# Optimization experiments

Measured on AMD Instinct MI355X. Metric: run time of the kernel, lower is better.

## Reference

```python
import jax, jax.numpy as jnp
import numpy as np

B, C, H, W = 16, 256, 64, 64
DIM = 8
HEADS = C // DIM          # 32
TD = HEADS * DIM          # 256 (total_dim)
EPS = 1e-15
BN_EPS = 1e-5


def setup_inputs() -> dict:
    key = jax.random.key(0)
    ks = jax.random.split(key, 7)
    s = 0.05
    return {
        "x": jax.random.normal(ks[0], (B, C, H, W), jnp.float32),
        "w_qkv": jax.random.normal(ks[1], (3 * TD, C), jnp.float32) * s,
        "w_dw": jax.random.normal(ks[2], (3 * TD, 1, 5, 5), jnp.float32) * s,
        "w_pw": jax.random.normal(ks[3], (3 * TD, DIM), jnp.float32) * s,
        "w_proj": jax.random.normal(ks[4], (C, 2 * TD), jnp.float32) * s,
        "bn_gamma": jnp.ones((C,), jnp.float32),
        "bn_beta": jnp.zeros((C,), jnp.float32),
        "bn_mean": jax.random.normal(ks[5], (C,), jnp.float32) * 0.1,
        "bn_var": jax.random.uniform(ks[6], (C,), jnp.float32, 0.5, 1.5),
    }


def reference(x, w_qkv, w_dw, w_pw, w_proj, bn_gamma, bn_beta, bn_mean, bn_var):
    # qkv: 1x1 conv, no bias -> (B, 3*TD, H, W)
    qkv = jnp.einsum('bchw,oc->bohw', x, w_qkv)

    # multi-scale aggregation: 5x5 depthwise conv then grouped 1x1 conv (groups = 3*HEADS)
    dw = jax.lax.conv_general_dilated(
        qkv, w_dw, window_strides=(1, 1), padding=[(2, 2), (2, 2)],
        dimension_numbers=('NCHW', 'OIHW', 'NCHW'), feature_group_count=3 * TD)
    G = 3 * HEADS                                   # groups; DIM channels per group
    dwg = dw.reshape(B, G, DIM, H, W)
    wg = w_pw.reshape(G, DIM, DIM)                  # (group, out_per_group, in_per_group)
    agg = jnp.einsum('bgihw,goi->bgohw', dwg, wg).reshape(B, 3 * TD, H, W)

    qkv_ms = jnp.concatenate([qkv, agg], axis=1)    # (B, 6*TD, H, W)

    # ReLU linear attention (H*W > dim branch)
    h2 = qkv_ms.shape[1] // (3 * DIM)               # 2*HEADS effective heads
    t = qkv_ms.reshape(B, h2, 3 * DIM, H * W)
    q = jax.nn.relu(t[:, :, :DIM])                  # (B,h2,DIM,N)
    k = jax.nn.relu(t[:, :, DIM:2 * DIM])           # (B,h2,DIM,N)
    v = t[:, :, 2 * DIM:]                           # (B,h2,DIM,N)
    v = jnp.concatenate([v, jnp.ones_like(v[:, :, :1])], axis=2)  # pad ones row -> (B,h2,DIM+1,N)

    vk = jnp.einsum('bhen,bhdn->bhed', v, k)        # (B,h2,DIM+1,DIM)
    out = jnp.einsum('bhed,bhdn->bhen', vk, q)      # (B,h2,DIM+1,N)
    out = out[:, :, :-1] / (out[:, :, -1:] + EPS)   # normalize by padded-ones channel
    out = out.reshape(B, h2 * DIM, H, W)            # (B, 2*TD, H, W)

    # proj: 1x1 conv + BatchNorm (inference stats)
    y = jnp.einsum('bchw,oc->bohw', out, w_proj)
    scale = (bn_gamma / jnp.sqrt(bn_var + BN_EPS))[None, :, None, None]
    y = (y - bn_mean[None, :, None, None]) * scale + bn_beta[None, :, None, None]

    return x + y
```

## Files before the change

### kernel.cpp

```cpp
#include <hip/hip_runtime.h>

#define BB 16
#define CC 256
#define HW 4096
#define TD3 768
#define TD2 512
#define WQ_N (TD3 * CC)
#define WP_N (CC * TD2)

typedef __bf16 bf16x8 __attribute__((ext_vector_type(8)));
typedef float f32x4 __attribute__((ext_vector_type(4)));
typedef const __attribute__((address_space(1))) unsigned int glb_u32;
typedef __attribute__((address_space(3))) unsigned int lds_u32;

__device__ inline ushort f2bf(float f) {
    union { float f; uint u; } v; v.f = f;
    uint u = v.u;
    return (ushort)((u + 0x7FFFu + ((u >> 16) & 1u)) >> 16);
}
__device__ inline float bf2f(ushort h) {
    union { uint u; float f; } v; v.u = ((uint)h) << 16;
    return v.f;
}
__device__ inline uint pack2(float a, float b) {
    return (uint)f2bf(a) | ((uint)f2bf(b) << 16);
}

__launch_bounds__(256)
__global__ void k_prep(const float* __restrict__ w_qkv, const float* __restrict__ w_proj,
                       ushort* __restrict__ wq_hi, ushort* __restrict__ wq_lo,
                       ushort* __restrict__ wp_hi, ushort* __restrict__ wp_lo) {
    int i = blockIdx.x * 256 + threadIdx.x;
    if (i < WQ_N) {
        float f = w_qkv[i];
        ushort h = f2bf(f);
        wq_hi[i] = h;
        wq_lo[i] = f2bf(f - bf2f(h));
    }
    if (i < WP_N) {
        float f = w_proj[i];
        ushort h = f2bf(f);
        wp_hi[i] = h;
        wp_lo[i] = f2bf(f - bf2f(h));
    }
}

__launch_bounds__(256)
__global__ void k0_transpose(const float* __restrict__ x, ushort* __restrict__ x_cl) {
    __shared__ float tile[64][65];
    int b = blockIdx.z;
    int n0 = blockIdx.x * 64;
    int c0 = blockIdx.y * 64;
    int t = threadIdx.x;
    const float* xp = x + ((size_t)b * CC + c0) * HW + n0;
    int nl = t & 63;
    int cl0 = t >> 6;
#pragma unroll
    for (int i = 0; i < 16; i++) {
        int cl = cl0 + i * 4;
        tile[cl][nl] = xp[(size_t)cl * HW + nl];
    }
    __syncthreads();
#pragma unroll
    for (int it = 0; it < 2; it++) {
        int item = t + it * 256;
        int n = item >> 3;
        int cc = item & 7;
        uint4 o;
        o.x = pack2(tile[cc * 8 + 0][n], tile[cc * 8 + 1][n]);
        o.y = pack2(tile[cc * 8 + 2][n], tile[cc * 8 + 3][n]);
        o.z = pack2(tile[cc * 8 + 4][n], tile[cc * 8 + 5][n]);
        o.w = pack2(tile[cc * 8 + 6][n], tile[cc * 8 + 7][n]);
        *(uint4*)(x_cl + ((size_t)b * HW + n0 + n) * CC + c0 + cc * 8) = o;
    }
}

__launch_bounds__(256)
__global__ void k1_qkv(const ushort* __restrict__ x_cl, const ushort* __restrict__ wq_hi,
                       const ushort* __restrict__ wq_lo, float* __restrict__ qkv_pl) {
    __shared__ ushort Ald[128][32];
    __shared__ ushort Bh[128][32];
    __shared__ ushort Bl[128][32];
    int b = blockIdx.z;
    int n0 = blockIdx.x * 128;
    int o0 = blockIdx.y * 128;
    int t = threadIdx.x;
    int w = t >> 6, l = t & 63;
    int wn = (w >> 1) * 64, wo = (w & 1) * 64;
    f32x4 acc[4][4];
#pragma unroll
    for (int m = 0; m < 4; m++)
#pragma unroll
        for (int o = 0; o < 4; o++)
#pragma unroll
            for (int r = 0; r < 4; r++) acc[m][o][r] = 0.f;

    const ushort* Ap  = x_cl + ((size_t)b * HW + n0) * CC;
    const ushort* Bph = wq_hi + (size_t)o0 * CC;
    const ushort* Bpl = wq_lo + (size_t)o0 * CC;
    int rowl = (l >> 2);
    int coll = (l & 3) * 8;

    for (int k0 = 0; k0 < CC; k0 += 32) {
#pragma unroll
        for (int i = 0; i < 2; i++) {
            int rbase = w * 32 + i * 16;
            int row = rbase + rowl;
            __builtin_amdgcn_global_load_lds((glb_u32*)(Ap + (size_t)row * CC + k0 + coll),
                                             (lds_u32*)&Ald[rbase][0], 16, 0, 0);
            __builtin_amdgcn_global_load_lds((glb_u32*)(Bph + (size_t)row * CC + k0 + coll),
                                             (lds_u32*)&Bh[rbase][0], 16, 0, 0);
            __builtin_amdgcn_global_load_lds((glb_u32*)(Bpl + (size_t)row * CC + k0 + coll),
                                             (lds_u32*)&Bl[rbase][0], 16, 0, 0);
        }
        __syncthreads();
        bf16x8 af[4], bh[4], bl[4];
#pragma unroll
        for (int m = 0; m < 4; m++) af[m] = *(const bf16x8*)&Ald[wn + m * 16 + (l & 15)][(l >> 4) * 8];
#pragma unroll
        for (int o = 0; o < 4; o++) {
            bh[o] = *(const bf16x8*)&Bh[wo + o * 16 + (l & 15)][(l >> 4) * 8];
            bl[o] = *(const bf16x8*)&Bl[wo + o * 16 + (l & 15)][(l >> 4) * 8];
        }
#pragma unroll
        for (int m = 0; m < 4; m++)
#pragma unroll
            for (int o = 0; o < 4; o++) {
                acc[m][o] = __builtin_amdgcn_mfma_f32_16x16x32_bf16(af[m], bh[o], acc[m][o], 0, 0, 0);
                acc[m][o] = __builtin_amdgcn_mfma_f32_16x16x32_bf16(af[m], bl[o], acc[m][o], 0, 0, 0);
            }
        __syncthreads();
    }
#pragma unroll
    for (int m = 0; m < 4; m++) {
        int nb = n0 + wn + m * 16 + (l >> 4) * 4;
#pragma unroll
        for (int oi = 0; oi < 4; oi++) {
            int o = o0 + wo + oi * 16 + (l & 15);
            float4 v4 = {acc[m][oi][0], acc[m][oi][1], acc[m][oi][2], acc[m][oi][3]};
            *(float4*)(qkv_pl + ((size_t)b * TD3 + o) * HW + nb) = v4;
        }
    }
}

__launch_bounds__(256)
__global__ void k2_dwpw(const float* __restrict__ qkv_pl, const float* __restrict__ w_dw,
                        const float* __restrict__ w_pw, float* __restrict__ agg_pl) {
    __shared__ __align__(16) float lds[2][36][76];
    int g = blockIdx.x;
    int strip = blockIdx.y;
    int b = blockIdx.z;
    int t = threadIdx.x;
    int y0 = strip * 32;
    const float* wg  = w_dw + (size_t)g * 200;
    const float* wpg = w_pw + (size_t)g * 64;
    const float* src = qkv_pl + ((size_t)b * TD3 + g * 8) * HW;
    float* dst = agg_pl + ((size_t)b * TD3 + g * 8) * HW;

    int rp = t >> 4;
    int seg = t & 15;

    int s_ch[5], s_row[5], s_q[5], s_ok[5];
#pragma unroll
    for (int i = 0; i < 5; i++) {
        int slot = t + i * 256;
        s_ok[i] = slot < 1152;
        int ch = slot / 576;
        int rem = slot - ch * 576;
        s_ch[i] = ch; s_row[i] = rem >> 4; s_q[i] = rem & 15;
    }

    if (t < 144) {
        int ch = t / 72, rem = t - ch * 72;
        int row = rem >> 1, side = rem & 1;
        float2 z2 = {0.f, 0.f};
        *(float2*)(&lds[ch][row][side ? 66 : 0]) = z2;
    }

    float4 sv[5];
#pragma unroll
    for (int i = 0; i < 5; i++) {
        float4 v = {0.f, 0.f, 0.f, 0.f};
        int yy = y0 - 2 + s_row[i];
        if (s_ok[i] && yy >= 0 && yy < 64)
            v = *(const float4*)(src + (size_t)s_ch[i] * HW + yy * 64 + s_q[i] * 4);
        sv[i] = v;
    }
#pragma unroll
    for (int i = 0; i < 5; i++) {
        if (s_ok[i]) {
            float2 lo2 = {sv[i].x, sv[i].y}, hi2 = {sv[i].z, sv[i].w};
            *(float2*)(&lds[s_ch[i]][s_row[i]][2 + 4 * s_q[i]]) = lo2;
            *(float2*)(&lds[s_ch[i]][s_row[i]][4 + 4 * s_q[i]]) = hi2;
        }
    }
    __syncthreads();

    float ag[8][8];
#pragma unroll
    for (int o = 0; o < 8; o++)
#pragma unroll
        for (int j = 0; j < 8; j++) ag[o][j] = 0.f;

#pragma unroll 1
    for (int cp = 0; cp < 4; cp++) {
        if (cp < 3) {
#pragma unroll
            for (int i = 0; i < 5; i++) {
                float4 v = {0.f, 0.f, 0.f, 0.f};
                int yy = y0 - 2 + s_row[i];
                if (s_ok[i] && yy >= 0 && yy < 64)
                    v = *(const float4*)(src + (size_t)(2 * (cp + 1) + s_ch[i]) * HW + yy * 64 + s_q[i] * 4);
                sv[i] = v;
            }
        }
#pragma unroll
        for (int ch = 0; ch < 2; ch++) {
            int c = cp * 2 + ch;
            float dw0[4] = {0.f, 0.f, 0.f, 0.f};
            float dw1[4] = {0.f, 0.f, 0.f, 0.f};
#pragma unroll
            for (int j = 0; j < 6; j++) {
                float win[8];
                *(float4*)&win[0] = *(const float4*)&lds[ch][rp * 2 + j][4 * seg];
                *(float4*)&win[4] = *(const float4*)&lds[ch][rp * 2 + j][4 * seg + 4];
                if (j <= 4) {
#pragma unroll
                    for (int dx = 0; dx < 5; dx++) {
                        float wv = wg[c * 25 + j * 5 + dx];
#pragma unroll
                        for (int k = 0; k < 4; k++) dw0[k] += win[dx + k] * wv;
                    }
                }
                if (j >= 1) {
#pragma unroll
                    for (int dx = 0; dx < 5; dx++) {
                        float wv = wg[c * 25 + (j - 1) * 5 + dx];
#pragma unroll
                        for (int k = 0; k < 4; k++) dw1[k] += win[dx + k] * wv;
                    }
                }
            }
#pragma unroll
            for (int o = 0; o < 8; o++) {
                float wv = wpg[o * 8 + c];
#pragma unroll
                for (int k = 0; k < 4; k++) {
                    ag[o][k] += dw0[k] * wv;
                    ag[o][4 + k] += dw1[k] * wv;
                }
            }
        }
        if (cp < 3) {
            __syncthreads();
#pragma unroll
            for (int i = 0; i < 5; i++) {
                if (s_ok[i]) {
                    float2 lo2 = {sv[i].x, sv[i].y}, hi2 = {sv[i].z, sv[i].w};
                    *(float2*)(&lds[s_ch[i]][s_row[i]][2 + 4 * s_q[i]]) = lo2;
                    *(float2*)(&lds[s_ch[i]][s_row[i]][4 + 4 * s_q[i]]) = hi2;
                }
            }
            __syncthreads();
        }
    }
    int n0 = (y0 + rp * 2) * 64 + seg * 4;
#pragma unroll
    for (int o = 0; o < 8; o++) {
        float4 r0 = {ag[o][0], ag[o][1], ag[o][2], ag[o][3]};
        float4 r1 = {ag[o][4], ag[o][5], ag[o][6], ag[o][7]};
        *(float4*)(dst + (size_t)o * HW + n0) = r0;
        *(float4*)(dst + (size_t)o * HW + n0 + 64) = r1;
    }
}

__launch_bounds__(256)
__global__ void k3_vk(const float* __restrict__ qkv_pl, const float* __restrict__ agg_pl,
                      float* __restrict__ vk_buf) {
    __shared__ float vk_partial[4][72];
    int h = blockIdx.x;
    int b = blockIdx.y;
    int s = blockIdx.z;
    const float* src = (h < 32) ? (qkv_pl + ((size_t)b * TD3 + h * 24) * HW)
                                : (agg_pl + ((size_t)b * TD3 + (h - 32) * 24) * HW);
    const float* kp = src + (size_t)8 * HW;
    const float* vp = src + (size_t)16 * HW;
    int t = threadIdx.x;
    float vk[9][8];
#pragma unroll
    for (int e = 0; e < 9; e++)
#pragma unroll
        for (int d = 0; d < 8; d++) vk[e][d] = 0.f;

#pragma unroll
    for (int it = 0; it < 2; it++) {
        int n4 = s * 2048 + (t + it * 256) * 4;
        float4 kf[8], vf[8];
#pragma unroll
        for (int d = 0; d < 8; d++) kf[d] = *(const float4*)(kp + (size_t)d * HW + n4);
#pragma unroll
        for (int e = 0; e < 8; e++) vf[e] = *(const float4*)(vp + (size_t)e * HW + n4);
#pragma unroll
        for (int d = 0; d < 8; d++) {
            kf[d].x = fmaxf(kf[d].x, 0.f); kf[d].y = fmaxf(kf[d].y, 0.f);
            kf[d].z = fmaxf(kf[d].z, 0.f); kf[d].w = fmaxf(kf[d].w, 0.f);
        }
#pragma unroll
        for (int e = 0; e < 8; e++)
#pragma unroll
            for (int d = 0; d < 8; d++)
                vk[e][d] += vf[e].x * kf[d].x + vf[e].y * kf[d].y + vf[e].z * kf[d].z + vf[e].w * kf[d].w;
#pragma unroll
        for (int d = 0; d < 8; d++) vk[8][d] += kf[d].x + kf[d].y + kf[d].z + kf[d].w;
    }
#pragma unroll
    for (int e = 0; e < 9; e++)
#pragma unroll
        for (int d = 0; d < 8; d++) {
            float v = vk[e][d];
            for (int off = 32; off > 0; off >>= 1) v += __shfl_xor(v, off);
            vk[e][d] = v;
        }
    int w = t >> 6, l = t & 63;
    if (l == 0) {
#pragma unroll
        for (int e = 0; e < 9; e++)
#pragma unroll
            for (int d = 0; d < 8; d++) vk_partial[w][e * 8 + d] = vk[e][d];
    }
    __syncthreads();
    if (t < 72) {
        float sum = vk_partial[0][t] + vk_partial[1][t] + vk_partial[2][t] + vk_partial[3][t];
        vk_buf[(((size_t)b * 64 + h) * 2 + s) * 72 + t] = sum;
    }
}

__launch_bounds__(256)
__global__ void k3_out(const float* __restrict__ qkv_pl, const float* __restrict__ agg_pl,
                       const float* __restrict__ vk_buf, ushort* __restrict__ out_cl) {
    __shared__ float vk_s[72];
    int h = blockIdx.x;
    int b = blockIdx.y;
    int s = blockIdx.z;
    const float* src = (h < 32) ? (qkv_pl + ((size_t)b * TD3 + h * 24) * HW)
                                : (agg_pl + ((size_t)b * TD3 + (h - 32) * 24) * HW);
    int t = threadIdx.x;
    if (t < 72) {
        const float* vb = vk_buf + ((size_t)b * 64 + h) * 2 * 72 + t;
        vk_s[t] = vb[0] + vb[72];
    }
    __syncthreads();
    float vkf[9][8];
#pragma unroll
    for (int e = 0; e < 9; e++)
#pragma unroll
        for (int d = 0; d < 8; d++) vkf[e][d] = vk_s[e * 8 + d];

    int n4 = s * 1024 + t * 4;
    float qa[4][8];
#pragma unroll
    for (int d = 0; d < 8; d++) {
        float4 q4 = *(const float4*)(src + (size_t)d * HW + n4);
        qa[0][d] = fmaxf(q4.x, 0.f); qa[1][d] = fmaxf(q4.y, 0.f);
        qa[2][d] = fmaxf(q4.z, 0.f); qa[3][d] = fmaxf(q4.w, 0.f);
    }
    ushort* dst = out_cl + (size_t)b * HW * TD2 + h * 8;
#pragma unroll
    for (int j = 0; j < 4; j++) {
        float o[9];
#pragma unroll
        for (int e = 0; e < 9; e++) {
            float sum = 0.f;
#pragma unroll
            for (int d = 0; d < 8; d++) sum += vkf[e][d] * qa[j][d];
            o[e] = sum;
        }
        float inv = 1.f / (o[8] + 1e-15f);
        uint4 ov;
        ov.x = pack2(o[0] * inv, o[1] * inv); ov.y = pack2(o[2] * inv, o[3] * inv);
        ov.z = pack2(o[4] * inv, o[5] * inv); ov.w = pack2(o[6] * inv, o[7] * inv);
        *(uint4*)(dst + (size_t)(n4 + j) * TD2) = ov;
    }
}

__launch_bounds__(256)
__global__ void k4_proj(const ushort* __restrict__ out_cl, const ushort* __restrict__ wp_hi,
                        const ushort* __restrict__ wp_lo, const float* __restrict__ x,
                        const float* __restrict__ gamma, const float* __restrict__ beta,
                        const float* __restrict__ mean, const float* __restrict__ var_,
                        float* __restrict__ out) {
    __shared__ ushort Ah[128][32];
    __shared__ ushort Al[128][32];
    __shared__ ushort Bld[128][32];
    int b = blockIdx.z;
    int n0 = blockIdx.x * 128;
    int c0 = blockIdx.y * 128;
    int t = threadIdx.x;
    int w = t >> 6, l = t & 63;
    int wc = (w >> 1) * 64, wn = (w & 1) * 64;
    f32x4 acc[4][4];
#pragma unroll
    for (int m = 0; m < 4; m++)
#pragma unroll
        for (int o = 0; o < 4; o++)
#pragma unroll
            for (int r = 0; r < 4; r++) acc[m][o][r] = 0.f;

    const ushort* Aph = wp_hi + (size_t)c0 * TD2;
    const ushort* Apl = wp_lo + (size_t)c0 * TD2;
    const ushort* Bp  = out_cl + ((size_t)b * HW + n0) * TD2;
    int rowl = (l >> 2);
    int coll = (l & 3) * 8;

    for (int k0 = 0; k0 < TD2; k0 += 32) {
#pragma unroll
        for (int i = 0; i < 2; i++) {
            int rbase = w * 32 + i * 16;
            int row = rbase + rowl;
            __builtin_amdgcn_global_load_lds((glb_u32*)(Aph + (size_t)row * TD2 + k0 + coll),
                                             (lds_u32*)&Ah[rbase][0], 16, 0, 0);
            __builtin_amdgcn_global_load_lds((glb_u32*)(Apl + (size_t)row * TD2 + k0 + coll),
                                             (lds_u32*)&Al[rbase][0], 16, 0, 0);
            __builtin_amdgcn_global_load_lds((glb_u32*)(Bp + (size_t)row * TD2 + k0 + coll),
                                             (lds_u32*)&Bld[rbase][0], 16, 0, 0);
        }
        __syncthreads();
        bf16x8 ah[4], al[4], bf[4];
#pragma unroll
        for (int m = 0; m < 4; m++) {
            ah[m] = *(const bf16x8*)&Ah[wc + m * 16 + (l & 15)][(l >> 4) * 8];
            al[m] = *(const bf16x8*)&Al[wc + m * 16 + (l & 15)][(l >> 4) * 8];
        }
#pragma unroll
        for (int ni = 0; ni < 4; ni++) bf[ni] = *(const bf16x8*)&Bld[wn + ni * 16 + (l & 15)][(l >> 4) * 8];
#pragma unroll
        for (int m = 0; m < 4; m++)
#pragma unroll
            for (int ni = 0; ni < 4; ni++) {
                acc[m][ni] = __builtin_amdgcn_mfma_f32_16x16x32_bf16(ah[m], bf[ni], acc[m][ni], 0, 0, 0);
                acc[m][ni] = __builtin_amdgcn_mfma_f32_16x16x32_bf16(al[m], bf[ni], acc[m][ni], 0, 0, 0);
            }
        __syncthreads();
    }
#pragma unroll
    for (int m = 0; m < 4; m++) {
        int cb = c0 + wc + m * 16 + (l >> 4) * 4;
        float sc[4], mn[4], bt[4];
#pragma unroll
        for (int r = 0; r < 4; r++) {
            sc[r] = gamma[cb + r] * rsqrtf(var_[cb + r] + 1e-5f);
            mn[r] = mean[cb + r];
            bt[r] = beta[cb + r];
        }
#pragma unroll
        for (int ni = 0; ni < 4; ni++) {
            int n = n0 + wn + ni * 16 + (l & 15);
#pragma unroll
            for (int r = 0; r < 4; r++) {
                size_t idx = ((size_t)b * CC + cb + r) * HW + n;
                out[idx] = x[idx] + (acc[m][ni][r] - mn[r]) * sc[r] + bt[r];
            }
        }
    }
}

extern "C" void kernel_launch(void* const* d_in, const int* in_sizes, int n_in,
                              void* d_out, int out_size, void* d_ws, size_t ws_size,
                              hipStream_t stream) {
    const float* x      = (const float*)d_in[0];
    const float* w_qkv  = (const float*)d_in[1];
    const float* w_dw   = (const float*)d_in[2];
    const float* w_pw   = (const float*)d_in[3];
    const float* w_proj = (const float*)d_in[4];
    const float* gamma  = (const float*)d_in[5];
    const float* beta   = (const float*)d_in[6];
    const float* mean   = (const float*)d_in[7];
    const float* var_   = (const float*)d_in[8];
    float* out = (float*)d_out;

    const size_t static_bytes = ((size_t)WQ_N + WP_N) * 2 * 2;
    const size_t per_batch = (size_t)HW * CC * 2 + (size_t)HW * TD3 * 4 * 2 + (size_t)HW * TD2 * 2
                           + (size_t)64 * 2 * 72 * 4;
    size_t avail = ws_size > static_bytes ? ws_size - static_bytes : 0;
    int cb = 16;
    while (cb > 1 && (size_t)cb * per_batch > avail) cb >>= 1;

    char* ws = (char*)d_ws;
    ushort* x_cl   = (ushort*)ws;
    float*  qkv_pl = (float*)(ws + (size_t)cb * HW * CC * 2);
    float*  agg_pl = (float*)(ws + (size_t)cb * HW * CC * 2 + (size_t)cb * HW * TD3 * 4);
    ushort* out_cl = (ushort*)(ws + (size_t)cb * HW * CC * 2 + (size_t)cb * HW * TD3 * 8);
    float*  vk_buf = (float*)(ws + (size_t)cb * HW * CC * 2 + (size_t)cb * HW * TD3 * 8
                                 + (size_t)cb * HW * TD2 * 2);
    char* wsw = ws + (size_t)cb * per_batch;
    ushort* wq_hi = (ushort*)wsw;
    ushort* wq_lo = wq_hi + WQ_N;
    ushort* wp_hi = wq_lo + WQ_N;
    ushort* wp_lo = wp_hi + WP_N;

    k_prep<<<dim3((WQ_N + 255) / 256), 256, 0, stream>>>(w_qkv, w_proj, wq_hi, wq_lo, wp_hi, wp_lo);

    for (int b0 = 0; b0 < BB; b0 += cb) {
        const float* xc = x + (size_t)b0 * CC * HW;
        float* oc = out + (size_t)b0 * CC * HW;
        k0_transpose<<<dim3(64, 4, cb), 256, 0, stream>>>(xc, x_cl);
        k1_qkv<<<dim3(32, 6, cb), 256, 0, stream>>>(x_cl, wq_hi, wq_lo, qkv_pl);
        k2_dwpw<<<dim3(96, 2, cb), 256, 0, stream>>>(qkv_pl, w_dw, w_pw, agg_pl);
        k3_vk<<<dim3(64, cb, 2), 256, 0, stream>>>(qkv_pl, agg_pl, vk_buf);
        k3_out<<<dim3(64, cb, 4), 256, 0, stream>>>(qkv_pl, agg_pl, vk_buf, out_cl);
        k4_proj<<<dim3(32, 2, cb), 256, 0, stream>>>(out_cl, wp_hi, wp_lo, xc, gamma, beta, mean, var_, oc);
    }
}
```

Measured before the change: 423.4 us.

## Store q/k intermediates in bf16 and split v into a separate fp32 buffer

The qkv projection output is split into a bf16 q/k plane buffer and an fp32 v plane buffer, and the depthwise/pointwise aggregation writes its outputs into the same split layouts. Downstream vk and output kernels read q and k as bf16, halving their memory traffic, while v stays fp32. This cuts global memory bandwidth across k1, k2, k3_vk and k3_out. The cost is reduced precision in q and k, which feed a ReLU attention with normalization, and extra branching in k2 on the channel type.

```diff
diff --git a/kernel.cpp b/kernel.cpp
--- a/kernel.cpp
+++ b/kernel.cpp
@@ -77,7 +77,8 @@
 
 __launch_bounds__(256)
 __global__ void k1_qkv(const ushort* __restrict__ x_cl, const ushort* __restrict__ wq_hi,
-                       const ushort* __restrict__ wq_lo, float* __restrict__ qkv_pl) {
+                       const ushort* __restrict__ wq_lo, ushort* __restrict__ qk_pl,
+                       float* __restrict__ v_pl) {
     __shared__ ushort Ald[128][32];
     __shared__ ushort Bh[128][32];
     __shared__ ushort Bl[128][32];
@@ -137,154 +138,212 @@
 #pragma unroll
         for (int oi = 0; oi < 4; oi++) {
             int o = o0 + wo + oi * 16 + (l & 15);
-            float4 v4 = {acc[m][oi][0], acc[m][oi][1], acc[m][oi][2], acc[m][oi][3]};
-            *(float4*)(qkv_pl + ((size_t)b * TD3 + o) * HW + nb) = v4;
-        }
-    }
-}
-
-__launch_bounds__(256)
-__global__ void k2_dwpw(const float* __restrict__ qkv_pl, const float* __restrict__ w_dw,
-                        const float* __restrict__ w_pw, float* __restrict__ agg_pl) {
-    __shared__ __align__(16) float lds[2][36][76];
+            int hl = o / 24;
+            int r = o - hl * 24;
+            if (r < 16) {
+                uint2 pv;
+                pv.x = pack2(acc[m][oi][0], acc[m][oi][1]);
+                pv.y = pack2(acc[m][oi][2], acc[m][oi][3]);
+                *(uint2*)(qk_pl + ((size_t)b * 1024 + hl * 16 + r) * HW + nb) = pv;
+            } else {
+                float4 v4 = {acc[m][oi][0], acc[m][oi][1], acc[m][oi][2], acc[m][oi][3]};
+                *(float4*)(v_pl + ((size_t)b * 512 + hl * 8 + (r - 16)) * HW + nb) = v4;
+            }
+        }
+    }
+}
+
+__launch_bounds__(256)
+__global__ void k2_dwpw(const ushort* __restrict__ qk_pl, const float* __restrict__ v_pl,
+                        const float* __restrict__ w_dw, const float* __restrict__ w_pw) {
+    __shared__ __align__(16) char ldsraw[2 * 36 * 76 * 4];
     int g = blockIdx.x;
     int strip = blockIdx.y;
     int b = blockIdx.z;
     int t = threadIdx.x;
     int y0 = strip * 32;
+    int hl = g / 3, tau = g % 3;
     const float* wg  = w_dw + (size_t)g * 200;
     const float* wpg = w_pw + (size_t)g * 64;
-    const float* src = qkv_pl + ((size_t)b * TD3 + g * 8) * HW;
-    float* dst = agg_pl + ((size_t)b * TD3 + g * 8) * HW;
-
     int rp = t >> 4;
     int seg = t & 15;
 
-    int s_ch[5], s_row[5], s_q[5], s_ok[5];
-#pragma unroll
-    for (int i = 0; i < 5; i++) {
-        int slot = t + i * 256;
-        s_ok[i] = slot < 1152;
-        int ch = slot / 576;
-        int rem = slot - ch * 576;
-        s_ch[i] = ch; s_row[i] = rem >> 4; s_q[i] = rem & 15;
-    }
-
-    if (t < 144) {
-        int ch = t / 72, rem = t - ch * 72;
-        int row = rem >> 1, side = rem & 1;
-        float2 z2 = {0.f, 0.f};
-        *(float2*)(&lds[ch][row][side ? 66 : 0]) = z2;
-    }
-
-    float4 sv[5];
-#pragma unroll
-    for (int i = 0; i < 5; i++) {
-        float4 v = {0.f, 0.f, 0.f, 0.f};
-        int yy = y0 - 2 + s_row[i];
-        if (s_ok[i] && yy >= 0 && yy < 64)
-            v = *(const float4*)(src + (size_t)s_ch[i] * HW + yy * 64 + s_q[i] * 4);
-        sv[i] = v;
-    }
-#pragma unroll
-    for (int i = 0; i < 5; i++) {
-        if (s_ok[i]) {
-            float2 lo2 = {sv[i].x, sv[i].y}, hi2 = {sv[i].z, sv[i].w};
-            *(float2*)(&lds[s_ch[i]][s_row[i]][2 + 4 * s_q[i]]) = lo2;
-            *(float2*)(&lds[s_ch[i]][s_row[i]][4 + 4 * s_q[i]]) = hi2;
-        }
-    }
-    __syncthreads();
-
     float ag[8][8];
 #pragma unroll
     for (int o = 0; o < 8; o++)
 #pragma unroll
         for (int j = 0; j < 8; j++) ag[o][j] = 0.f;
 
+    if (tau < 2) {
+        typedef ushort (*ltile_t)[36][72];
+        ltile_t lds = (ltile_t)ldsraw;
+        const ushort* src = qk_pl + ((size_t)b * 1024 + hl * 16 + tau * 8) * HW;
+        ushort* dst = (ushort*)qk_pl + ((size_t)b * 1024 + 512 + hl * 16 + tau * 8) * HW;
+        if (t < 72) {
+            int ch = t / 36, row = t - ch * 36;
+            *(uint*)(&lds[ch][row][0]) = 0u;
+            *(uint*)(&lds[ch][row][66]) = 0u;
+        }
 #pragma unroll 1
-    for (int cp = 0; cp < 4; cp++) {
-        if (cp < 3) {
-#pragma unroll
-            for (int i = 0; i < 5; i++) {
-                float4 v = {0.f, 0.f, 0.f, 0.f};
-                int yy = y0 - 2 + s_row[i];
-                if (s_ok[i] && yy >= 0 && yy < 64)
-                    v = *(const float4*)(src + (size_t)(2 * (cp + 1) + s_ch[i]) * HW + yy * 64 + s_q[i] * 4);
-                sv[i] = v;
-            }
-        }
-#pragma unroll
-        for (int ch = 0; ch < 2; ch++) {
-            int c = cp * 2 + ch;
-            float dw0[4] = {0.f, 0.f, 0.f, 0.f};
-            float dw1[4] = {0.f, 0.f, 0.f, 0.f};
-#pragma unroll
-            for (int j = 0; j < 6; j++) {
-                float win[8];
-                *(float4*)&win[0] = *(const float4*)&lds[ch][rp * 2 + j][4 * seg];
-                *(float4*)&win[4] = *(const float4*)&lds[ch][rp * 2 + j][4 * seg + 4];
-                if (j <= 4) {
-#pragma unroll
-                    for (int dx = 0; dx < 5; dx++) {
-                        float wv = wg[c * 25 + j * 5 + dx];
-#pragma unroll
-                        for (int k = 0; k < 4; k++) dw0[k] += win[dx + k] * wv;
+        for (int cp = 0; cp < 4; cp++) {
+            if (cp) __syncthreads();
+#pragma unroll
+            for (int i = 0; i < 3; i++) {
+                int slot = t + i * 256;
+                if (slot < 576) {
+                    int ch = slot / 288;
+                    int rem = slot - ch * 288;
+                    int row = rem >> 3;
+                    int q = rem & 7;
+                    int yy = y0 - 2 + row;
+                    uint4 v = {0u, 0u, 0u, 0u};
+                    if (yy >= 0 && yy < 64)
+                        v = *(const uint4*)(src + (size_t)(2 * cp + ch) * HW + yy * 64 + q * 8);
+                    ushort* rowp = &lds[ch][row][2 + q * 8];
+                    *(uint*)(rowp + 0) = v.x; *(uint*)(rowp + 2) = v.y;
+                    *(uint*)(rowp + 4) = v.z; *(uint*)(rowp + 6) = v.w;
+                }
+            }
+            __syncthreads();
+#pragma unroll
+            for (int ch = 0; ch < 2; ch++) {
+                int c = cp * 2 + ch;
+                float dw0[4] = {0.f, 0.f, 0.f, 0.f};
+                float dw1[4] = {0.f, 0.f, 0.f, 0.f};
+#pragma unroll
+                for (int j = 0; j < 6; j++) {
+                    ushort4 wa = *(const ushort4*)&lds[ch][rp * 2 + j][4 * seg];
+                    ushort4 wb = *(const ushort4*)&lds[ch][rp * 2 + j][4 * seg + 4];
+                    float win[8];
+                    win[0] = bf2f(wa.x); win[1] = bf2f(wa.y); win[2] = bf2f(wa.z); win[3] = bf2f(wa.w);
+                    win[4] = bf2f(wb.x); win[5] = bf2f(wb.y); win[6] = bf2f(wb.z); win[7] = bf2f(wb.w);
+                    if (j <= 4) {
+#pragma unroll
+                        for (int dx = 0; dx < 5; dx++) {
+                            float wv = wg[c * 25 + j * 5 + dx];
+#pragma unroll
+                            for (int k = 0; k < 4; k++) dw0[k] += win[dx + k] * wv;
+                        }
+                    }
+                    if (j >= 1) {
+#pragma unroll
+                        for (int dx = 0; dx < 5; dx++) {
+                            float wv = wg[c * 25 + (j - 1) * 5 + dx];
+#pragma unroll
+                            for (int k = 0; k < 4; k++) dw1[k] += win[dx + k] * wv;
+                        }
                     }
                 }
-                if (j >= 1) {
-#pragma unroll
-                    for (int dx = 0; dx < 5; dx++) {
-                        float wv = wg[c * 25 + (j - 1) * 5 + dx];
-#pragma unroll
-                        for (int k = 0; k < 4; k++) dw1[k] += win[dx + k] * wv;
+#pragma unroll
+                for (int o = 0; o < 8; o++) {
+                    float wv = wpg[o * 8 + c];
+#pragma unroll
+                    for (int k = 0; k < 4; k++) {
+                        ag[o][k] += dw0[k] * wv;
+                        ag[o][4 + k] += dw1[k] * wv;
                     }
                 }
             }
-#pragma unroll
-            for (int o = 0; o < 8; o++) {
-                float wv = wpg[o * 8 + c];
-#pragma unroll
-                for (int k = 0; k < 4; k++) {
-                    ag[o][k] += dw0[k] * wv;
-                    ag[o][4 + k] += dw1[k] * wv;
+        }
+        int n0 = (y0 + rp * 2) * 64 + seg * 4;
+#pragma unroll
+        for (int o = 0; o < 8; o++) {
+            uint2 r0, r1;
+            r0.x = pack2(ag[o][0], ag[o][1]); r0.y = pack2(ag[o][2], ag[o][3]);
+            r1.x = pack2(ag[o][4], ag[o][5]); r1.y = pack2(ag[o][6], ag[o][7]);
+            *(uint2*)(dst + (size_t)o * HW + n0) = r0;
+            *(uint2*)(dst + (size_t)o * HW + n0 + 64) = r1;
+        }
+    } else {
+        typedef float (*ltile_t)[36][76];
+        ltile_t lds = (ltile_t)ldsraw;
+        const float* src = v_pl + ((size_t)b * 512 + hl * 8) * HW;
+        float* dst = (float*)v_pl + ((size_t)b * 512 + 256 + hl * 8) * HW;
+        if (t < 144) {
+            int ch = t / 72, rem = t - ch * 72;
+            int row = rem >> 1, side = rem & 1;
+            float2 z2 = {0.f, 0.f};
+            *(float2*)(&lds[ch][row][side ? 66 : 0]) = z2;
+        }
+#pragma unroll 1
+        for (int cp = 0; cp < 4; cp++) {
+            if (cp) __syncthreads();
+#pragma unroll
+            for (int i = 0; i < 5; i++) {
+                int slot = t + i * 256;
+                if (slot < 1152) {
+                    int ch = slot / 576;
+                    int rem = slot - ch * 576;
+                    int row = rem >> 4;
+                    int q = rem & 15;
+                    int yy = y0 - 2 + row;
+                    float4 v = {0.f, 0.f, 0.f, 0.f};
+                    if (yy >= 0 && yy < 64)
+                        v = *(const float4*)(src + (size_t)(2 * cp + ch) * HW + yy * 64 + q * 4);
+                    float2 lo2 = {v.x, v.y}, hi2 = {v.z, v.w};
+                    *(float2*)(&lds[ch][row][2 + 4 * q]) = lo2;
+                    *(float2*)(&lds[ch][row][4 + 4 * q]) = hi2;
                 }
             }
-        }
-        if (cp < 3) {
             __syncthreads();
 #pragma unroll
-            for (int i = 0; i < 5; i++) {
-                if (s_ok[i]) {
-                    float2 lo2 = {sv[i].x, sv[i].y}, hi2 = {sv[i].z, sv[i].w};
-                    *(float2*)(&lds[s_ch[i]][s_row[i]][2 + 4 * s_q[i]]) = lo2;
-                    *(float2*)(&lds[s_ch[i]][s_row[i]][4 + 4 * s_q[i]]) = hi2;
+            for (int ch = 0; ch < 2; ch++) {
+                int c = cp * 2 + ch;
+                float dw0[4] = {0.f, 0.f, 0.f, 0.f};
+                float dw1[4] = {0.f, 0.f, 0.f, 0.f};
+#pragma unroll
+                for (int j = 0; j < 6; j++) {
+                    float win[8];
+                    *(float4*)&win[0] = *(const float4*)&lds[ch][rp * 2 + j][4 * seg];
+                    *(float4*)&win[4] = *(const float4*)&lds[ch][rp * 2 + j][4 * seg + 4];
+                    if (j <= 4) {
+#pragma unroll
+                        for (int dx = 0; dx < 5; dx++) {
+                            float wv = wg[c * 25 + j * 5 + dx];
+#pragma unroll
+                            for (int k = 0; k < 4; k++) dw0[k] += win[dx + k] * wv;
+                        }
+                    }
+                    if (j >= 1) {
+#pragma unroll
+                        for (int dx = 0; dx < 5; dx++) {
+                            float wv = wg[c * 25 + (j - 1) * 5 + dx];
+#pragma unroll
+                            for (int k = 0; k < 4; k++) dw1[k] += win[dx + k] * wv;
+                        }
+                    }
                 }
-            }
-            __syncthreads();
-        }
-    }
-    int n0 = (y0 + rp * 2) * 64 + seg * 4;
-#pragma unroll
-    for (int o = 0; o < 8; o++) {
-        float4 r0 = {ag[o][0], ag[o][1], ag[o][2], ag[o][3]};
-        float4 r1 = {ag[o][4], ag[o][5], ag[o][6], ag[o][7]};
-        *(float4*)(dst + (size_t)o * HW + n0) = r0;
-        *(float4*)(dst + (size_t)o * HW + n0 + 64) = r1;
-    }
-}
-
-__launch_bounds__(256)
-__global__ void k3_vk(const float* __restrict__ qkv_pl, const float* __restrict__ agg_pl,
+#pragma unroll
+                for (int o = 0; o < 8; o++) {
+                    float wv = wpg[o * 8 + c];
+#pragma unroll
+                    for (int k = 0; k < 4; k++) {
+                        ag[o][k] += dw0[k] * wv;
+                        ag[o][4 + k] += dw1[k] * wv;
+                    }
+                }
+            }
+        }
+        int n0 = (y0 + rp * 2) * 64 + seg * 4;
+#pragma unroll
+        for (int o = 0; o < 8; o++) {
+            float4 r0 = {ag[o][0], ag[o][1], ag[o][2], ag[o][3]};
+            float4 r1 = {ag[o][4], ag[o][5], ag[o][6], ag[o][7]};
+            *(float4*)(dst + (size_t)o * HW + n0) = r0;
+            *(float4*)(dst + (size_t)o * HW + n0 + 64) = r1;
+        }
+    }
+}
+
+__launch_bounds__(256)
+__global__ void k3_vk(const ushort* __restrict__ qk_pl, const float* __restrict__ v_pl,
                       float* __restrict__ vk_buf) {
     __shared__ float vk_partial[4][72];
     int h = blockIdx.x;
     int b = blockIdx.y;
     int s = blockIdx.z;
-    const float* src = (h < 32) ? (qkv_pl + ((size_t)b * TD3 + h * 24) * HW)
-                                : (agg_pl + ((size_t)b * TD3 + (h - 32) * 24) * HW);
-    const float* kp = src + (size_t)8 * HW;
-    const float* vp = src + (size_t)16 * HW;
+    const ushort* kp = qk_pl + ((size_t)b * 1024 + (h >> 5) * 512 + (h & 31) * 16 + 8) * HW;
+    const float*  vp = v_pl  + ((size_t)b * 512  + (h >> 5) * 256 + (h & 31) * 8) * HW;
     int t = threadIdx.x;
     float vk[9][8];
 #pragma unroll
@@ -297,14 +356,13 @@
         int n4 = s * 2048 + (t + it * 256) * 4;
         float4 kf[8], vf[8];
 #pragma unroll
-        for (int d = 0; d < 8; d++) kf[d] = *(const float4*)(kp + (size_t)d * HW + n4);
+        for (int d = 0; d < 8; d++) {
+            ushort4 ku = *(const ushort4*)(kp + (size_t)d * HW + n4);
+            kf[d].x = fmaxf(bf2f(ku.x), 0.f); kf[d].y = fmaxf(bf2f(ku.y), 0.f);
+            kf[d].z = fmaxf(bf2f(ku.z), 0.f); kf[d].w = fmaxf(bf2f(ku.w), 0.f);
+        }
 #pragma unroll
         for (int e = 0; e < 8; e++) vf[e] = *(const float4*)(vp + (size_t)e * HW + n4);
-#pragma unroll
-        for (int d = 0; d < 8; d++) {
-            kf[d].x = fmaxf(kf[d].x, 0.f); kf[d].y = fmaxf(kf[d].y, 0.f);
-            kf[d].z = fmaxf(kf[d].z, 0.f); kf[d].w = fmaxf(kf[d].w, 0.f);
-        }
 #pragma unroll
         for (int e = 0; e < 8; e++)
 #pragma unroll
@@ -336,14 +394,13 @@
 }
 
 __launch_bounds__(256)
-__global__ void k3_out(const float* __restrict__ qkv_pl, const float* __restrict__ agg_pl,
-                       const float* __restrict__ vk_buf, ushort* __restrict__ out_cl) {
+__global__ void k3_out(const ushort* __restrict__ qk_pl, const float* __restrict__ vk_buf,
+                       ushort* __restrict__ out_cl) {
     __shared__ float vk_s[72];
     int h = blockIdx.x;
     int b = blockIdx.y;
     int s = blockIdx.z;
-    const float* src = (h < 32) ? (qkv_pl + ((size_t)b * TD3 + h * 24) * HW)
-                                : (agg_pl + ((size_t)b * TD3 + (h - 32) * 24) * HW);
+    const ushort* qp = qk_pl + ((size_t)b * 1024 + (h >> 5) * 512 + (h & 31) * 16) * HW;
     int t = threadIdx.x;
     if (t < 72) {
         const float* vb = vk_buf + ((size_t)b * 64 + h) * 2 * 72 + t;
@@ -360,9 +417,9 @@
     float qa[4][8];
 #pragma unroll
     for (int d = 0; d < 8; d++) {
-        float4 q4 = *(const float4*)(src + (size_t)d * HW + n4);
-        qa[0][d] = fmaxf(q4.x, 0.f); qa[1][d] = fmaxf(q4.y, 0.f);
-        qa[2][d] = fmaxf(q4.z, 0.f); qa[3][d] = fmaxf(q4.w, 0.f);
+        ushort4 qu = *(const ushort4*)(qp + (size_t)d * HW + n4);
+        qa[0][d] = fmaxf(bf2f(qu.x), 0.f); qa[1][d] = fmaxf(bf2f(qu.y), 0.f);
+        qa[2][d] = fmaxf(bf2f(qu.z), 0.f); qa[3][d] = fmaxf(bf2f(qu.w), 0.f);
     }
     ushort* dst = out_cl + (size_t)b * HW * TD2 + h * 8;
 #pragma unroll
@@ -479,19 +536,20 @@
     float* out = (float*)d_out;
 
     const size_t static_bytes = ((size_t)WQ_N + WP_N) * 2 * 2;
-    const size_t per_batch = (size_t)HW * CC * 2 + (size_t)HW * TD3 * 4 * 2 + (size_t)HW * TD2 * 2
-                           + (size_t)64 * 2 * 72 * 4;
+    const size_t per_batch = (size_t)HW * CC * 2 + (size_t)1024 * HW * 2 + (size_t)512 * HW * 4
+                           + (size_t)HW * TD2 * 2 + (size_t)64 * 2 * 72 * 4;
     size_t avail = ws_size > static_bytes ? ws_size - static_bytes : 0;
     int cb = 16;
     while (cb > 1 && (size_t)cb * per_batch > avail) cb >>= 1;
 
     char* ws = (char*)d_ws;
-    ushort* x_cl   = (ushort*)ws;
-    float*  qkv_pl = (float*)(ws + (size_t)cb * HW * CC * 2);
-    float*  agg_pl = (float*)(ws + (size_t)cb * HW * CC * 2 + (size_t)cb * HW * TD3 * 4);
-    ushort* out_cl = (ushort*)(ws + (size_t)cb * HW * CC * 2 + (size_t)cb * HW * TD3 * 8);
-    float*  vk_buf = (float*)(ws + (size_t)cb * HW * CC * 2 + (size_t)cb * HW * TD3 * 8
-                                 + (size_t)cb * HW * TD2 * 2);
+    ushort* x_cl  = (ushort*)ws;
+    ushort* qk_pl = (ushort*)(ws + (size_t)cb * HW * CC * 2);
+    float*  v_pl  = (float*)(ws + (size_t)cb * HW * CC * 2 + (size_t)cb * 1024 * HW * 2);
+    ushort* out_cl = (ushort*)(ws + (size_t)cb * HW * CC * 2 + (size_t)cb * 1024 * HW * 2
+                                  + (size_t)cb * 512 * HW * 4);
+    float*  vk_buf = (float*)(ws + (size_t)cb * HW * CC * 2 + (size_t)cb * 1024 * HW * 2
+                                 + (size_t)cb * 512 * HW * 4 + (size_t)cb * HW * TD2 * 2);
     char* wsw = ws + (size_t)cb * per_batch;
     ushort* wq_hi = (ushort*)wsw;
     ushort* wq_lo = wq_hi + WQ_N;
@@ -504,10 +562,10 @@
         const float* xc = x + (size_t)b0 * CC * HW;
         float* oc = out + (size_t)b0 * CC * HW;
         k0_transpose<<<dim3(64, 4, cb), 256, 0, stream>>>(xc, x_cl);
-        k1_qkv<<<dim3(32, 6, cb), 256, 0, stream>>>(x_cl, wq_hi, wq_lo, qkv_pl);
-        k2_dwpw<<<dim3(96, 2, cb), 256, 0, stream>>>(qkv_pl, w_dw, w_pw, agg_pl);
-        k3_vk<<<dim3(64, cb, 2), 256, 0, stream>>>(qkv_pl, agg_pl, vk_buf);
-        k3_out<<<dim3(64, cb, 4), 256, 0, stream>>>(qkv_pl, agg_pl, vk_buf, out_cl);
+        k1_qkv<<<dim3(32, 6, cb), 256, 0, stream>>>(x_cl, wq_hi, wq_lo, qk_pl, v_pl);
+        k2_dwpw<<<dim3(96, 2, cb), 256, 0, stream>>>(qk_pl, v_pl, w_dw, w_pw);
+        k3_vk<<<dim3(64, cb, 2), 256, 0, stream>>>(qk_pl, v_pl, vk_buf);
+        k3_out<<<dim3(64, cb, 4), 256, 0, stream>>>(qk_pl, vk_buf, out_cl);
         k4_proj<<<dim3(32, 2, cb), 256, 0, stream>>>(out_cl, wp_hi, wp_lo, xc, gamma, beta, mean, var_, oc);
     }
 }
```

Result: faster. 391.1 us (-7.6%).
